# Kernel tuning notes

Measured on AMD Instinct MI355X. Metric: run time of the kernel, lower is better.

Reference implementation:

```python
import jax, jax.numpy as jnp
import numpy as np

ENC_DIM, DEC_DIM, ATT_DIM = 2048, 512, 512
BATCH, NPIX = 256, 196


def setup_inputs() -> dict:
    key = jax.random.key(0)
    ks = jax.random.split(key, 8)
    s = lambda d: 1.0 / np.sqrt(d)
    return {
        "encoder_out": jax.random.normal(ks[0], (BATCH, NPIX, ENC_DIM), jnp.float32),
        "decoder_hidden": jax.random.normal(ks[1], (BATCH, DEC_DIM), jnp.float32),
        "W_enc": jax.random.uniform(ks[2], (ENC_DIM, ATT_DIM), jnp.float32, -s(ENC_DIM), s(ENC_DIM)),
        "b_enc": jax.random.uniform(ks[3], (ATT_DIM,), jnp.float32, -s(ENC_DIM), s(ENC_DIM)),
        "W_dec": jax.random.uniform(ks[4], (DEC_DIM, ATT_DIM), jnp.float32, -s(DEC_DIM), s(DEC_DIM)),
        "b_dec": jax.random.uniform(ks[5], (ATT_DIM,), jnp.float32, -s(DEC_DIM), s(DEC_DIM)),
        "w_full": jax.random.uniform(ks[6], (ATT_DIM,), jnp.float32, -s(ATT_DIM), s(ATT_DIM)),
        "b_full": jax.random.uniform(ks[7], (), jnp.float32, -s(ATT_DIM), s(ATT_DIM)),
    }


def reference(encoder_out, decoder_hidden, W_enc, b_enc, W_dec, b_dec, w_full, b_full):
    # att1: (B, P, A); att2: (B, 1, A)
    att1 = jnp.einsum('bpe,ea->bpa', encoder_out, W_enc) + b_enc
    att2 = (decoder_hidden @ W_dec + b_dec)[:, None, :]
    # score: (B, P) via full_att projecting A -> 1
    att = jnp.einsum('bpa,a->bp', jax.nn.relu(att1 + att2), w_full) + b_full
    alpha = jax.nn.softmax(att, axis=1)
    context = jnp.einsum('bpe,bp->be', encoder_out, alpha)
    return context, alpha
```

## Files before the change

kernel.cpp:

```cpp
#include <hip/hip_runtime.h>
#include <hip/hip_bf16.h>

#define ENC_DIM 2048
#define DEC_DIM 512
#define ATT_DIM 512
#define BATCH   256
#define NPIX    196

typedef __attribute__((ext_vector_type(8)))  short short8;
typedef __attribute__((ext_vector_type(16))) float f32x16;

__device__ __forceinline__ short f2bf(float x) {
    unsigned u = __builtin_bit_cast(unsigned, x);
    unsigned r = (u + 0x7FFFu + ((u >> 16) & 1u)) >> 16;
    return (short)r;
}

__global__ __launch_bounds__(256) void bahdanau_prep(
    const float* __restrict__ dec_h, const float* __restrict__ W_enc,
    const float* __restrict__ b_enc, const float* __restrict__ W_dec,
    const float* __restrict__ b_dec,
    float* __restrict__ att2pb, short* __restrict__ Wpack)
{
    int blk = blockIdx.x;
    if (blk < BATCH) {
        __shared__ float hs[DEC_DIM];
        int b = blk;
        for (int i = threadIdx.x; i < DEC_DIM; i += 256) hs[i] = dec_h[b * DEC_DIM + i];
        __syncthreads();
        for (int a = threadIdx.x; a < ATT_DIM; a += 256) {
            float s = 0.f;
            #pragma unroll 8
            for (int d = 0; d < DEC_DIM; ++d) s += hs[d] * W_dec[d * ATT_DIM + a];
            att2pb[b * ATT_DIM + a] = s + b_dec[a] + b_enc[a];
        }
    } else {
        int c    = (blk - BATCH) * 256 + threadIdx.x;
        int lane = c & 63;
        int kb16 = (c >> 6) & 127;
        int nt   = c >> 13;
        int n     = nt * 32 + (lane & 31);
        int kbase = kb16 * 16 + (lane >> 5) * 8;
        short8 v;
        #pragma unroll
        for (int j = 0; j < 8; ++j) v[j] = f2bf(W_enc[(kbase + j) * ATT_DIM + n]);
        *reinterpret_cast<short8*>(Wpack + (size_t)c * 8) = v;
    }
}

__global__ __launch_bounds__(512) void bahdanau_main(
    const float* __restrict__ enc, const float* __restrict__ w_full,
    const float* __restrict__ att2pb, const short* __restrict__ Wpack,
    float* __restrict__ out_ctx, float* __restrict__ out_alpha)
{
    __shared__ __align__(16) short Bs[8 * 4 * 64 * 8];
    __shared__ float red[264];

    const int b    = blockIdx.x;
    const int tid  = threadIdx.x;
    const int lane = tid & 63;
    const int wid  = tid >> 6;

    const float* encB = enc + (size_t)b * NPIX * ENC_DIM;

    const int arow  = wid * 32 + (lane & 31);
    const int arowc = arow < NPIX ? arow : NPIX - 1;
    const float* aptr = encB + (size_t)arowc * ENC_DIM + (lane >> 5) * 8;

    float sp[16];
    #pragma unroll
    for (int r = 0; r < 16; ++r) sp[r] = 0.f;

    for (int nc = 0; nc < 2; ++nc) {
        f32x16 acc[8];
        #pragma unroll
        for (int t = 0; t < 8; ++t)
            #pragma unroll
            for (int r = 0; r < 16; ++r) acc[t][r] = 0.f;

        for (int kb = 0; kb < ENC_DIM / 64; ++kb) {
            __syncthreads();
            {
                const short8* src = reinterpret_cast<const short8*>(Wpack);
                short8*       dst = reinterpret_cast<short8*>(Bs);
                #pragma unroll
                for (int i = 0; i < 4; ++i) {
                    int idx = tid + i * 512;
                    int c   = idx >> 6;
                    int ln  = idx & 63;
                    int nt   = nc * 8 + (c >> 2);
                    int kb16 = kb * 4 + (c & 3);
                    dst[idx] = src[(nt * 128 + kb16) * 64 + ln];
                }
            }
            __syncthreads();
            #pragma unroll
            for (int kk = 0; kk < 4; ++kk) {
                const float* ap = aptr + kb * 64 + kk * 16;
                float4 f0 = *reinterpret_cast<const float4*>(ap);
                float4 f1 = *reinterpret_cast<const float4*>(ap + 4);
                short8 afr;
                afr[0] = f2bf(f0.x); afr[1] = f2bf(f0.y);
                afr[2] = f2bf(f0.z); afr[3] = f2bf(f0.w);
                afr[4] = f2bf(f1.x); afr[5] = f2bf(f1.y);
                afr[6] = f2bf(f1.z); afr[7] = f2bf(f1.w);
                #pragma unroll
                for (int t = 0; t < 8; ++t) {
                    short8 bfr = *reinterpret_cast<const short8*>(
                        Bs + ((t * 4 + kk) * 64 + lane) * 8);
                    acc[t] = __builtin_amdgcn_mfma_f32_32x32x16_bf16(afr, bfr, acc[t], 0, 0, 0);
                }
            }
        }
        #pragma unroll
        for (int t = 0; t < 8; ++t) {
            int col  = nc * 256 + t * 32 + (lane & 31);
            float c2 = att2pb[b * ATT_DIM + col];
            float wf = w_full[col];
            #pragma unroll
            for (int r = 0; r < 16; ++r) {
                float v = acc[t][r] + c2;
                v = v > 0.f ? v : 0.f;
                sp[r] += v * wf;
            }
        }
    }

    #pragma unroll
    for (int r = 0; r < 16; ++r) {
        float v = sp[r];
        v += __shfl_xor(v, 1);
        v += __shfl_xor(v, 2);
        v += __shfl_xor(v, 4);
        v += __shfl_xor(v, 8);
        v += __shfl_xor(v, 16);
        sp[r] = v;
    }
    if ((lane & 31) == 0) {
        #pragma unroll
        for (int r = 0; r < 16; ++r) {
            int p = wid * 32 + (r & 3) + 8 * (r >> 2) + 4 * (lane >> 5);
            red[p] = sp[r];
        }
    }
    __syncthreads();

    if (wid == 0) {
        float s0 = red[lane], s1 = red[lane + 64], s2 = red[lane + 128];
        float s3 = (lane < NPIX - 192) ? red[lane + 192] : -3.4e38f;
        float m = fmaxf(fmaxf(s0, s1), fmaxf(s2, s3));
        #pragma unroll
        for (int d = 1; d <= 32; d <<= 1) m = fmaxf(m, __shfl_xor(m, d));
        float e = __expf(s0 - m) + __expf(s1 - m) + __expf(s2 - m)
                + ((lane < NPIX - 192) ? __expf(s3 - m) : 0.f);
        #pragma unroll
        for (int d = 1; d <= 32; d <<= 1) e += __shfl_xor(e, d);
        if (lane == 0) { red[256] = m; red[257] = e; }
    }
    __syncthreads();
    float m    = red[256];
    float rinv = 1.f / red[257];
    if (tid < NPIX) {
        float a = __expf(red[tid] - m) * rinv;
        red[tid] = a;
        out_alpha[b * NPIX + tid] = a;
    }
    __syncthreads();

    float4 ctx = {0.f, 0.f, 0.f, 0.f};
    const float4* enc4 = reinterpret_cast<const float4*>(encB);
    for (int p = 0; p < NPIX; ++p) {
        float a  = red[p];
        float4 v = enc4[p * (ENC_DIM / 4) + tid];
        ctx.x += a * v.x; ctx.y += a * v.y; ctx.z += a * v.z; ctx.w += a * v.w;
    }
    reinterpret_cast<float4*>(out_ctx)[(size_t)b * (ENC_DIM / 4) + tid] = ctx;
}

extern "C" void kernel_launch(void* const* d_in, const int* in_sizes, int n_in,
                              void* d_out, int out_size, void* d_ws, size_t ws_size,
                              hipStream_t stream) {
    const float* enc    = (const float*)d_in[0];
    const float* dech   = (const float*)d_in[1];
    const float* W_enc  = (const float*)d_in[2];
    const float* b_enc  = (const float*)d_in[3];
    const float* W_dec  = (const float*)d_in[4];
    const float* b_dec  = (const float*)d_in[5];
    const float* w_full = (const float*)d_in[6];

    float* att2pb = (float*)d_ws;
    short* Wpack  = (short*)((char*)d_ws + 512 * 1024);

    float* out_ctx   = (float*)d_out;
    float* out_alpha = out_ctx + (size_t)BATCH * ENC_DIM;

    bahdanau_prep<<<768, 256, 0, stream>>>(dech, W_enc, b_enc, W_dec, b_dec, att2pb, Wpack);
    bahdanau_main<<<BATCH, 512, 0, stream>>>(enc, w_full, att2pb, Wpack, out_ctx, out_alpha);
}
```

Before: 363.8 us.

## Split main kernel into parallel GEMM tiles plus separate softmax/context kernel

The fused per-batch kernel is split in two. A GEMM kernel runs 1024 blocks, each covering one (batch, row-half, column-half) tile, and stages W through double-buffered LDS using direct global-to-LDS loads. A second kernel sums the partial scores, applies the softmax and computes the context. This raises the grid from 256 to 1024 blocks and overlaps the staging of W with MFMA work. In exchange it adds a kernel launch and a workspace round trip for the scores, and the A tiles are now read twice, once per column half.

```diff
diff --git a/kernel.cpp b/kernel.cpp
--- a/kernel.cpp
+++ b/kernel.cpp
@@ -9,6 +9,9 @@
 
 typedef __attribute__((ext_vector_type(8)))  short short8;
 typedef __attribute__((ext_vector_type(16))) float f32x16;
+
+typedef const __attribute__((address_space(1))) unsigned int gu32;
+typedef __attribute__((address_space(3))) unsigned int lu32;
 
 __device__ __forceinline__ short f2bf(float x) {
     unsigned u = __builtin_bit_cast(unsigned, x);
@@ -48,84 +51,93 @@
     }
 }
 
-__global__ __launch_bounds__(512) void bahdanau_main(
+__global__ __launch_bounds__(512, 4) void bahdanau_gemm(
     const float* __restrict__ enc, const float* __restrict__ w_full,
     const float* __restrict__ att2pb, const short* __restrict__ Wpack,
-    float* __restrict__ out_ctx, float* __restrict__ out_alpha)
+    float* __restrict__ spart)
 {
-    __shared__ __align__(16) short Bs[8 * 4 * 64 * 8];
-    __shared__ float red[264];
-
-    const int b    = blockIdx.x;
+    __shared__ __align__(16) short Bs[2][16384];
+    __shared__ float red[2][128];
+
+    const int f  = blockIdx.x;
+    const int nc = (f >> 3) & 1;
+    const int pp = (f >> 4) * 8 + (f & 7);
+    const int b  = pp >> 1, rh = pp & 1;
+
     const int tid  = threadIdx.x;
     const int lane = tid & 63;
     const int wid  = tid >> 6;
+    const int rt   = wid & 3;
+    const int g    = wid >> 2;
 
     const float* encB = enc + (size_t)b * NPIX * ENC_DIM;
-
-    const int arow  = wid * 32 + (lane & 31);
-    const int arowc = arow < NPIX ? arow : NPIX - 1;
-    const float* aptr = encB + (size_t)arowc * ENC_DIM + (lane >> 5) * 8;
+    int grow = rh * 128 + rt * 32 + (lane & 31);
+    if (grow > NPIX - 1) grow = NPIX - 1;
+    const float* aptr = encB + (size_t)grow * ENC_DIM + ((lane >> 5) << 3);
+
+    const short8* Wc = reinterpret_cast<const short8*>(Wpack);
+
+    f32x16 acc[4];
+    #pragma unroll
+    for (int t = 0; t < 4; ++t)
+        #pragma unroll
+        for (int r = 0; r < 16; ++r) acc[t][r] = 0.f;
+
+    auto STAGE = [&](int buf, int kb) {
+        #pragma unroll
+        for (int i = 0; i < 4; ++i) {
+            int idx = tid + i * 512;
+            int c   = idx >> 6;
+            int ln  = idx & 63;
+            int nt   = nc * 8 + (c >> 2);
+            int kb16 = kb * 4 + (c & 3);
+            const void* gp = (const void*)(Wc + (size_t)(nt * 128 + kb16) * 64 + ln);
+            void*       lp = (void*)(&Bs[buf][idx * 8]);
+            __builtin_amdgcn_global_load_lds((gu32*)gp, (lu32*)lp, 16, 0, 0);
+        }
+    };
+
+    STAGE(0, 0);
+    for (int kb = 0; kb < ENC_DIM / 64; ++kb) {
+        int cur = kb & 1;
+        __syncthreads();
+        if (kb < ENC_DIM / 64 - 1) STAGE(cur ^ 1, kb + 1);
+        const short* Bb = &Bs[cur][0];
+        #pragma unroll
+        for (int kk = 0; kk < 4; ++kk) {
+            const float* ap = aptr + kb * 64 + kk * 16;
+            float4 f0 = *reinterpret_cast<const float4*>(ap);
+            float4 f1 = *reinterpret_cast<const float4*>(ap + 4);
+            short8 afr;
+            afr[0] = f2bf(f0.x); afr[1] = f2bf(f0.y);
+            afr[2] = f2bf(f0.z); afr[3] = f2bf(f0.w);
+            afr[4] = f2bf(f1.x); afr[5] = f2bf(f1.y);
+            afr[6] = f2bf(f1.z); afr[7] = f2bf(f1.w);
+            #pragma unroll
+            for (int t = 0; t < 4; ++t) {
+                int tt = g * 4 + t;
+                short8 bfr = *reinterpret_cast<const short8*>(
+                    Bb + ((tt * 4 + kk) * 64 + lane) * 8);
+                acc[t] = __builtin_amdgcn_mfma_f32_32x32x16_bf16(afr, bfr, acc[t], 0, 0, 0);
+            }
+        }
+    }
 
     float sp[16];
     #pragma unroll
     for (int r = 0; r < 16; ++r) sp[r] = 0.f;
-
-    for (int nc = 0; nc < 2; ++nc) {
-        f32x16 acc[8];
-        #pragma unroll
-        for (int t = 0; t < 8; ++t)
-            #pragma unroll
-            for (int r = 0; r < 16; ++r) acc[t][r] = 0.f;
-
-        for (int kb = 0; kb < ENC_DIM / 64; ++kb) {
-            __syncthreads();
-            {
-                const short8* src = reinterpret_cast<const short8*>(Wpack);
-                short8*       dst = reinterpret_cast<short8*>(Bs);
-                #pragma unroll
-                for (int i = 0; i < 4; ++i) {
-                    int idx = tid + i * 512;
-                    int c   = idx >> 6;
-                    int ln  = idx & 63;
-                    int nt   = nc * 8 + (c >> 2);
-                    int kb16 = kb * 4 + (c & 3);
-                    dst[idx] = src[(nt * 128 + kb16) * 64 + ln];
-                }
-            }
-            __syncthreads();
-            #pragma unroll
-            for (int kk = 0; kk < 4; ++kk) {
-                const float* ap = aptr + kb * 64 + kk * 16;
-                float4 f0 = *reinterpret_cast<const float4*>(ap);
-                float4 f1 = *reinterpret_cast<const float4*>(ap + 4);
-                short8 afr;
-                afr[0] = f2bf(f0.x); afr[1] = f2bf(f0.y);
-                afr[2] = f2bf(f0.z); afr[3] = f2bf(f0.w);
-                afr[4] = f2bf(f1.x); afr[5] = f2bf(f1.y);
-                afr[6] = f2bf(f1.z); afr[7] = f2bf(f1.w);
-                #pragma unroll
-                for (int t = 0; t < 8; ++t) {
-                    short8 bfr = *reinterpret_cast<const short8*>(
-                        Bs + ((t * 4 + kk) * 64 + lane) * 8);
-                    acc[t] = __builtin_amdgcn_mfma_f32_32x32x16_bf16(afr, bfr, acc[t], 0, 0, 0);
-                }
-            }
-        }
-        #pragma unroll
-        for (int t = 0; t < 8; ++t) {
-            int col  = nc * 256 + t * 32 + (lane & 31);
-            float c2 = att2pb[b * ATT_DIM + col];
-            float wf = w_full[col];
-            #pragma unroll
-            for (int r = 0; r < 16; ++r) {
-                float v = acc[t][r] + c2;
-                v = v > 0.f ? v : 0.f;
-                sp[r] += v * wf;
-            }
-        }
-    }
-
+    #pragma unroll
+    for (int t = 0; t < 4; ++t) {
+        int col  = nc * 256 + g * 128 + t * 32 + (lane & 31);
+        float c2 = att2pb[b * ATT_DIM + col];
+        float wf = w_full[col];
+        #pragma unroll
+        for (int r = 0; r < 16; ++r) {
+            float v = acc[t][r] + c2;
+            v = v > 0.f ? v : 0.f;
+            sp[r] += v * wf;
+        }
+    }
     #pragma unroll
     for (int r = 0; r < 16; ++r) {
         float v = sp[r];
@@ -139,42 +151,64 @@
     if ((lane & 31) == 0) {
         #pragma unroll
         for (int r = 0; r < 16; ++r) {
-            int p = wid * 32 + (r & 3) + 8 * (r >> 2) + 4 * (lane >> 5);
-            red[p] = sp[r];
-        }
-    }
+            int lr = rt * 32 + (r & 3) + 8 * (r >> 2) + 4 * (lane >> 5);
+            red[g][lr] = sp[r];
+        }
+    }
+    __syncthreads();
+    if (tid < 128) {
+        int p = rh * 128 + tid;
+        if (p < NPIX)
+            spart[nc * (BATCH * 224) + b * 224 + p] = red[0][tid] + red[1][tid];
+    }
+}
+
+__global__ __launch_bounds__(512) void bahdanau_ctx(
+    const float* __restrict__ enc, const float* __restrict__ spart,
+    float* __restrict__ out_ctx, float* __restrict__ out_alpha)
+{
+    __shared__ float al[256];
+    __shared__ float msum[2];
+    const int b    = blockIdx.x;
+    const int tid  = threadIdx.x;
+    const int lane = tid & 63;
+    const int wid  = tid >> 6;
+
+    if (tid < NPIX)
+        al[tid] = spart[b * 224 + tid] + spart[BATCH * 224 + b * 224 + tid];
+    else if (tid < 256)
+        al[tid] = -3.4e38f;
     __syncthreads();
 
     if (wid == 0) {
-        float s0 = red[lane], s1 = red[lane + 64], s2 = red[lane + 128];
-        float s3 = (lane < NPIX - 192) ? red[lane + 192] : -3.4e38f;
+        float s0 = al[lane], s1 = al[lane + 64], s2 = al[lane + 128], s3 = al[lane + 192];
         float m = fmaxf(fmaxf(s0, s1), fmaxf(s2, s3));
         #pragma unroll
         for (int d = 1; d <= 32; d <<= 1) m = fmaxf(m, __shfl_xor(m, d));
-        float e = __expf(s0 - m) + __expf(s1 - m) + __expf(s2 - m)
-                + ((lane < NPIX - 192) ? __expf(s3 - m) : 0.f);
+        float e = __expf(s0 - m) + __expf(s1 - m) + __expf(s2 - m) + __expf(s3 - m);
         #pragma unroll
         for (int d = 1; d <= 32; d <<= 1) e += __shfl_xor(e, d);
-        if (lane == 0) { red[256] = m; red[257] = e; }
-    }
-    __syncthreads();
-    float m    = red[256];
-    float rinv = 1.f / red[257];
+        if (lane == 0) { msum[0] = m; msum[1] = e; }
+    }
+    __syncthreads();
+    float m    = msum[0];
+    float rinv = 1.f / msum[1];
     if (tid < NPIX) {
-        float a = __expf(red[tid] - m) * rinv;
-        red[tid] = a;
+        float a = __expf(al[tid] - m) * rinv;
+        al[tid] = a;
         out_alpha[b * NPIX + tid] = a;
     }
     __syncthreads();
 
-    float4 ctx = {0.f, 0.f, 0.f, 0.f};
-    const float4* enc4 = reinterpret_cast<const float4*>(encB);
+    float4 c4 = {0.f, 0.f, 0.f, 0.f};
+    const float4* enc4 = reinterpret_cast<const float4*>(enc + (size_t)b * NPIX * ENC_DIM);
+    #pragma unroll 4
     for (int p = 0; p < NPIX; ++p) {
-        float a  = red[p];
-        float4 v = enc4[p * (ENC_DIM / 4) + tid];
-        ctx.x += a * v.x; ctx.y += a * v.y; ctx.z += a * v.z; ctx.w += a * v.w;
-    }
-    reinterpret_cast<float4*>(out_ctx)[(size_t)b * (ENC_DIM / 4) + tid] = ctx;
+        float a  = al[p];
+        float4 v = enc4[(size_t)p * (ENC_DIM / 4) + tid];
+        c4.x += a * v.x; c4.y += a * v.y; c4.z += a * v.z; c4.w += a * v.w;
+    }
+    reinterpret_cast<float4*>(out_ctx)[(size_t)b * (ENC_DIM / 4) + tid] = c4;
 }
 
 extern "C" void kernel_launch(void* const* d_in, const int* in_sizes, int n_in,
@@ -190,10 +224,12 @@
 
     float* att2pb = (float*)d_ws;
     short* Wpack  = (short*)((char*)d_ws + 512 * 1024);
+    float* spart  = (float*)((char*)d_ws + 2560 * 1024);
 
     float* out_ctx   = (float*)d_out;
     float* out_alpha = out_ctx + (size_t)BATCH * ENC_DIM;
 
     bahdanau_prep<<<768, 256, 0, stream>>>(dech, W_enc, b_enc, W_dec, b_dec, att2pb, Wpack);
-    bahdanau_main<<<BATCH, 512, 0, stream>>>(enc, w_full, att2pb, Wpack, out_ctx, out_alpha);
-}
+    bahdanau_gemm<<<1024, 512, 0, stream>>>(enc, w_full, att2pb, Wpack, spart);
+    bahdanau_ctx<<<BATCH, 512, 0, stream>>>(enc, spart, out_ctx, out_alpha);
+}
```

After: 447.9 us. 1.23x slower.
